# Kernel optimization log

Hardware: AMD Instinct MI355X
Metric: run time of the kernel (lower is better)

Reference implementation:

```python
import jax, jax.numpy as jnp
import numpy as np

# Module config (matches init_kwargs)
IN_F = 4096
OUT_F = 12288
R = 16
ENABLE_LORA = [True, False, True]
N_BLOCKS = len(ENABLE_LORA)          # 3 fused output blocks (Q, K, V)
GROUPS = sum(ENABLE_LORA)            # 2 LoRA-enabled blocks
OUT_PG = OUT_F // N_BLOCKS           # 4096 rows per block
ENABLED_IDX = np.array([i for i, e in enumerate(ENABLE_LORA) if e])  # [0, 2]


def setup_inputs() -> dict:
    key = jax.random.key(0)
    kx, ka, kb = jax.random.split(key, 3)
    x = jax.random.normal(kx, (2, 512, IN_F), dtype=jnp.float32)
    # kaiming_uniform-like scale is irrelevant for correctness testing; use randn
    weight_A = jax.random.normal(ka, (GROUPS * R, IN_F), dtype=jnp.float32) * 0.02
    weight_B = jax.random.normal(kb, (OUT_PG * GROUPS, R), dtype=jnp.float32) * 0.02
    return {"x": x, "weight_A": weight_A, "weight_B": weight_B}


def _merge_AB(weight_A, weight_B):
    # grouped conv1d with kernel size 1 == per-group matmul B_g @ A_g
    A = weight_A.reshape(GROUPS, R, IN_F)          # (g, r, in)
    B = weight_B.reshape(GROUPS, OUT_PG, R)        # (g, out_pg, r)
    delta = jnp.einsum('gor,gri->goi', B, A)       # (g, out_pg, in)
    # zero_pad: scatter enabled blocks into the full (N_BLOCKS, out_pg, in) weight
    W = jnp.zeros((N_BLOCKS, OUT_PG, IN_F), dtype=delta.dtype)
    W = W.at[jnp.asarray(ENABLED_IDX)].set(delta)
    return W.reshape(OUT_F, IN_F)


def reference(x, weight_A, weight_B):
    W = _merge_AB(weight_A, weight_B)              # (out_f, in_f), full materialization as in torch
    return jnp.einsum('bsi,oi->bso', x, W)         # F.linear(x, W), no bias (lora_bias=False)
```

## Files before the change

kernel.cpp:

```cpp
#include <hip/hip_runtime.h>
#include <hip/hip_bf16.h>

#define IN_F   4096
#define OUT_F  12288
#define OUT_PG 4096
#define M_ROWS 1024
#define R2     32

template <int KS>
__global__ __launch_bounds__(256) void lora_a_kernel(
    const float* __restrict__ x, const float* __restrict__ wA,
    float* __restrict__ Tpart) {
  constexpr int SLICE  = IN_F / KS;
  constexpr int CHUNKS = SLICE / 256;
  __shared__ float As[R2 * 256];

  const int t = threadIdx.x;
  const int l = t & 63;
  const int w = t >> 6;
  const int ks = blockIdx.x;
  const int row0 = blockIdx.y * 8 + w * 2;
  const int kb = ks * SLICE;

  float acc[2][32];
#pragma unroll
  for (int m = 0; m < 2; ++m)
#pragma unroll
    for (int r = 0; r < 32; ++r) acc[m][r] = 0.f;

  for (int c = 0; c < CHUNKS; ++c) {
    const int kc = kb + c * 256;
    if (c) __syncthreads();
#pragma unroll
    for (int i = 0; i < 8; ++i) {
      const int f = t * 4 + i * 1024;
      const int r = f >> 8, kk = f & 255;
      *reinterpret_cast<float4*>(&As[f]) =
          *reinterpret_cast<const float4*>(&wA[r * IN_F + kc + kk]);
    }
    __syncthreads();

    float4 xv[2];
#pragma unroll
    for (int m = 0; m < 2; ++m)
      xv[m] = *reinterpret_cast<const float4*>(&x[(row0 + m) * IN_F + kc + l * 4]);

#pragma unroll
    for (int r = 0; r < 32; ++r) {
      const float4 av = *reinterpret_cast<const float4*>(&As[r * 256 + l * 4]);
      acc[0][r] += xv[0].x * av.x + xv[0].y * av.y + xv[0].z * av.z + xv[0].w * av.w;
      acc[1][r] += xv[1].x * av.x + xv[1].y * av.y + xv[1].z * av.z + xv[1].w * av.w;
    }
  }

  float v[2];
#pragma unroll
  for (int m2 = 0; m2 < 2; ++m2) {
#pragma unroll
    for (int m = 16; m >= 1; m >>= 1) {
#pragma unroll
      for (int i = 0; i < m; ++i) {
        const float a = acc[m2][i], b = acc[m2][i + m];
        const float mine   = (l & m) ? b : a;
        const float theirs = (l & m) ? a : b;
        acc[m2][i] = mine + __shfl_xor(theirs, m, 64);
      }
    }
    v[m2] = acc[m2][0] + __shfl_xor(acc[m2][0], 32, 64);
  }
  const float outv = (l < 32) ? v[0] : v[1];
  Tpart[(ks * M_ROWS + row0 + (l >> 5)) * R2 + (l & 31)] = outv;
}

template <int KS>
__global__ __launch_bounds__(256) void lora_b_kernel(
    const float* __restrict__ Tpart, const float* __restrict__ wB,
    float* __restrict__ out) {
  const int t = threadIdx.x;
  const int bx = blockIdx.x;
  const int by = blockIdx.y;
  const int cbase = bx << 8;
  const int rbase = by << 7;
  const int outblk = bx >> 4;
  const int cq = t & 63;
  const int rowg = t >> 6;
  const int col = cbase + cq * 4;

  if (outblk == 1) {
    const float4 z = {0.f, 0.f, 0.f, 0.f};
#pragma unroll
    for (int rr = 0; rr < 32; ++rr) {
      const int row = rbase + rowg * 32 + rr;
      *reinterpret_cast<float4*>(&out[row * OUT_F + col]) = z;
    }
    return;
  }
  const int g = outblk >> 1;
  const int jbase = cbase - ((outblk == 2) ? 2 * OUT_PG : 0);

  __shared__ float BsT[16 * 260];
  __shared__ float Ts[128 * 16];

#pragma unroll
  for (int i = 0; i < 4; ++i) {
    const int idx = t + i * 256;
    const int c = idx >> 2, r0 = (idx & 3) * 4;
    const float4 v = *reinterpret_cast<const float4*>(
        &wB[(g * OUT_PG + jbase + c) * 16 + r0]);
    BsT[(r0 + 0) * 260 + c] = v.x;
    BsT[(r0 + 1) * 260 + c] = v.y;
    BsT[(r0 + 2) * 260 + c] = v.z;
    BsT[(r0 + 3) * 260 + c] = v.w;
  }
#pragma unroll
  for (int i = 0; i < 2; ++i) {
    const int idx = t + i * 256;
    const int row = idx >> 2, q = idx & 3;
    float4 s = {0.f, 0.f, 0.f, 0.f};
#pragma unroll
    for (int ks = 0; ks < KS; ++ks) {
      const float4 vv = *reinterpret_cast<const float4*>(
          &Tpart[(ks * M_ROWS + rbase + row) * R2 + g * 16 + q * 4]);
      s.x += vv.x; s.y += vv.y; s.z += vv.z; s.w += vv.w;
    }
    *reinterpret_cast<float4*>(&Ts[row * 16 + q * 4]) = s;
  }
  __syncthreads();

  float4 brow[16];
#pragma unroll
  for (int r = 0; r < 16; ++r)
    brow[r] = *reinterpret_cast<const float4*>(&BsT[r * 260 + cq * 4]);

#pragma unroll
  for (int rr = 0; rr < 32; ++rr) {
    const int rowl = rowg * 32 + rr;
    float ts[16];
#pragma unroll
    for (int q = 0; q < 4; ++q)
      *reinterpret_cast<float4*>(&ts[q * 4]) =
          *reinterpret_cast<const float4*>(&Ts[rowl * 16 + q * 4]);
    float a0 = 0.f, a1 = 0.f, a2 = 0.f, a3 = 0.f;
#pragma unroll
    for (int r = 0; r < 16; ++r) {
      a0 += ts[r] * brow[r].x;
      a1 += ts[r] * brow[r].y;
      a2 += ts[r] * brow[r].z;
      a3 += ts[r] * brow[r].w;
    }
    const float4 accv = {a0, a1, a2, a3};
    *reinterpret_cast<float4*>(&out[(rbase + rowl) * OUT_F + col]) = accv;
  }
}

extern "C" void kernel_launch(void* const* d_in, const int* in_sizes, int n_in,
                              void* d_out, int out_size, void* d_ws, size_t ws_size,
                              hipStream_t stream) {
  const float* x  = (const float*)d_in[0];
  const float* wA = (const float*)d_in[1];
  const float* wB = (const float*)d_in[2];
  float* out = (float*)d_out;
  float* Tpart = (float*)d_ws;

  const size_t ws_elems = ws_size / sizeof(float);
  if (ws_elems >= (size_t)16 * M_ROWS * R2) {
    lora_a_kernel<16><<<dim3(16, M_ROWS / 8), 256, 0, stream>>>(x, wA, Tpart);
    lora_b_kernel<16><<<dim3(OUT_F / 256, M_ROWS / 128), 256, 0, stream>>>(Tpart, wB, out);
  } else if (ws_elems >= (size_t)8 * M_ROWS * R2) {
    lora_a_kernel<8><<<dim3(8, M_ROWS / 8), 256, 0, stream>>>(x, wA, Tpart);
    lora_b_kernel<8><<<dim3(OUT_F / 256, M_ROWS / 128), 256, 0, stream>>>(Tpart, wB, out);
  } else {
    lora_a_kernel<4><<<dim3(4, M_ROWS / 8), 256, 0, stream>>>(x, wA, Tpart);
    lora_b_kernel<4><<<dim3(OUT_F / 256, M_ROWS / 128), 256, 0, stream>>>(Tpart, wB, out);
  }
}
```

Measured before the change: 98.08 us.

## Move zero-block stores into LoRA-A kernel and shrink B-kernel row tiles

Zero-filling of the disabled middle output block moves out of the B kernel and into the A kernel, where each block writes a slice of zeros alongside its reduction work. The B kernel now launches only over the two enabled blocks and uses 32-row tiles instead of 128, giving four times as many blocks with less serial work each. The aim is to overlap the zero-store bandwidth with the latency-bound A computation and to raise occupancy in the B kernel. In exchange, wB is reloaded into shared memory by more blocks and the A kernel carries extra store traffic.

```diff
diff --git a/kernel.cpp b/kernel.cpp
--- a/kernel.cpp
+++ b/kernel.cpp
@@ -10,9 +10,10 @@
 template <int KS>
 __global__ __launch_bounds__(256) void lora_a_kernel(
     const float* __restrict__ x, const float* __restrict__ wA,
-    float* __restrict__ Tpart) {
+    float* __restrict__ Tpart, float* __restrict__ out) {
   constexpr int SLICE  = IN_F / KS;
   constexpr int CHUNKS = SLICE / 256;
+  constexpr int ZC     = OUT_PG / KS;
   __shared__ float As[R2 * 256];
 
   const int t = threadIdx.x;
@@ -21,6 +22,19 @@
   const int ks = blockIdx.x;
   const int row0 = blockIdx.y * 8 + w * 2;
   const int kb = ks * SLICE;
+
+  {
+    const int zrow0 = blockIdx.y * 8;
+    const int zcol0 = OUT_PG + ks * ZC;
+    const float4 z = {0.f, 0.f, 0.f, 0.f};
+#pragma unroll
+    for (int i = 0; i < ZC / 128; ++i) {
+      const int idx = t + i * 256;
+      const int zr = idx / (ZC / 4);
+      const int zc = (idx % (ZC / 4)) * 4;
+      *reinterpret_cast<float4*>(&out[(zrow0 + zr) * OUT_F + zcol0 + zc]) = z;
+    }
+  }
 
   float acc[2][32];
 #pragma unroll
@@ -79,27 +93,15 @@
   const int t = threadIdx.x;
   const int bx = blockIdx.x;
   const int by = blockIdx.y;
-  const int cbase = bx << 8;
-  const int rbase = by << 7;
-  const int outblk = bx >> 4;
+  const int g = bx >> 4;
+  const int jbase = (bx & 15) << 8;
+  const int colbase = g ? (2 * OUT_PG + jbase) : jbase;
+  const int rbase = by << 5;
   const int cq = t & 63;
   const int rowg = t >> 6;
-  const int col = cbase + cq * 4;
-
-  if (outblk == 1) {
-    const float4 z = {0.f, 0.f, 0.f, 0.f};
-#pragma unroll
-    for (int rr = 0; rr < 32; ++rr) {
-      const int row = rbase + rowg * 32 + rr;
-      *reinterpret_cast<float4*>(&out[row * OUT_F + col]) = z;
-    }
-    return;
-  }
-  const int g = outblk >> 1;
-  const int jbase = cbase - ((outblk == 2) ? 2 * OUT_PG : 0);
 
   __shared__ float BsT[16 * 260];
-  __shared__ float Ts[128 * 16];
+  __shared__ float Ts[32 * 16];
 
 #pragma unroll
   for (int i = 0; i < 4; ++i) {
@@ -112,10 +114,8 @@
     BsT[(r0 + 2) * 260 + c] = v.z;
     BsT[(r0 + 3) * 260 + c] = v.w;
   }
-#pragma unroll
-  for (int i = 0; i < 2; ++i) {
-    const int idx = t + i * 256;
-    const int row = idx >> 2, q = idx & 3;
+  if (t < 128) {
+    const int row = t >> 2, q = t & 3;
     float4 s = {0.f, 0.f, 0.f, 0.f};
 #pragma unroll
     for (int ks = 0; ks < KS; ++ks) {
@@ -133,8 +133,8 @@
     brow[r] = *reinterpret_cast<const float4*>(&BsT[r * 260 + cq * 4]);
 
 #pragma unroll
-  for (int rr = 0; rr < 32; ++rr) {
-    const int rowl = rowg * 32 + rr;
+  for (int rr = 0; rr < 8; ++rr) {
+    const int rowl = rowg * 8 + rr;
     float ts[16];
 #pragma unroll
     for (int q = 0; q < 4; ++q)
@@ -149,7 +149,7 @@
       a3 += ts[r] * brow[r].w;
     }
     const float4 accv = {a0, a1, a2, a3};
-    *reinterpret_cast<float4*>(&out[(rbase + rowl) * OUT_F + col]) = accv;
+    *reinterpret_cast<float4*>(&out[(rbase + rowl) * OUT_F + colbase + cq * 4]) = accv;
   }
 }
 
@@ -164,13 +164,13 @@
 
   const size_t ws_elems = ws_size / sizeof(float);
   if (ws_elems >= (size_t)16 * M_ROWS * R2) {
-    lora_a_kernel<16><<<dim3(16, M_ROWS / 8), 256, 0, stream>>>(x, wA, Tpart);
-    lora_b_kernel<16><<<dim3(OUT_F / 256, M_ROWS / 128), 256, 0, stream>>>(Tpart, wB, out);
+    lora_a_kernel<16><<<dim3(16, M_ROWS / 8), 256, 0, stream>>>(x, wA, Tpart, out);
+    lora_b_kernel<16><<<dim3(32, M_ROWS / 32), 256, 0, stream>>>(Tpart, wB, out);
   } else if (ws_elems >= (size_t)8 * M_ROWS * R2) {
-    lora_a_kernel<8><<<dim3(8, M_ROWS / 8), 256, 0, stream>>>(x, wA, Tpart);
-    lora_b_kernel<8><<<dim3(OUT_F / 256, M_ROWS / 128), 256, 0, stream>>>(Tpart, wB, out);
+    lora_a_kernel<8><<<dim3(8, M_ROWS / 8), 256, 0, stream>>>(x, wA, Tpart, out);
+    lora_b_kernel<8><<<dim3(32, M_ROWS / 32), 256, 0, stream>>>(Tpart, wB, out);
   } else {
-    lora_a_kernel<4><<<dim3(4, M_ROWS / 8), 256, 0, stream>>>(x, wA, Tpart);
-    lora_b_kernel<4><<<dim3(OUT_F / 256, M_ROWS / 128), 256, 0, stream>>>(Tpart, wB, out);
+    lora_a_kernel<4><<<dim3(4, M_ROWS / 8), 256, 0, stream>>>(x, wA, Tpart, out);
+    lora_b_kernel<4><<<dim3(32, M_ROWS / 32), 256, 0, stream>>>(Tpart, wB, out);
   }
 }
```

New measurement: 94.59 us. 1.04x faster.
